# Performance work log

Measured on AMD Instinct MI355X. Metric: run time of the kernel, lower is better.

The kernel has to match this reference:

```python
import jax, jax.numpy as jnp
import numpy as np

F8 = jnp.float8_e4m3fn
F8_MAX = 448.0  # finfo(float8_e4m3fn).max

def setup_inputs() -> dict:
    key = jax.random.key(0)
    k1, k2, k3 = jax.random.split(key, 3)
    B, S, IN, OUT = 4, 4096, 2048, 2048
    x = jax.random.normal(k1, (B, S, IN), dtype=jnp.float32)
    # Pre-quantized fp8 weight [OUT, IN] with a per-tensor scale, as stored by AutoFP8
    w = jax.random.normal(k2, (OUT, IN), dtype=jnp.float32)
    weight_scale = (jnp.max(jnp.abs(w)) / F8_MAX).astype(jnp.float32)
    qweight = jnp.clip(w / weight_scale, -F8_MAX, F8_MAX).astype(F8)
    input_scale = jnp.asarray(0.05, dtype=jnp.float32)  # static activation scale
    bias = jax.random.normal(k3, (OUT,), dtype=jnp.float32)
    return {"x": x, "qweight": qweight, "weight_scale": weight_scale,
            "input_scale": input_scale, "bias": bias}

def reference(x, qweight, weight_scale, input_scale, bias):
    # per_tensor_quantize: divide by static scale, clamp to fp8 range, cast to e4m3fn
    qinput = jnp.clip(x / input_scale, -F8_MAX, F8_MAX).astype(F8)  # [B,S,IN] fp8
    # scaled fp8 GEMM with fused dequant + bias epilogue (out_dtype = x.dtype)
    a = qinput.astype(x.dtype) * input_scale          # dequant activations
    b = qweight.astype(x.dtype) * weight_scale        # dequant weights [OUT,IN]
    return jnp.einsum('bsi,oi->bso', a, b) + bias     # [B,S,OUT]
```

## Files before the change

kernel.cpp:

```cpp
#include <hip/hip_runtime.h>
#include <stdint.h>

typedef float  floatx4 __attribute__((ext_vector_type(4)));
typedef int    intx4   __attribute__((ext_vector_type(4)));
typedef int    intx8   __attribute__((ext_vector_type(8)));

#define AS1 __attribute__((address_space(1)))
#define AS3 __attribute__((address_space(3)))

__device__ __forceinline__ float quant_e4m3_value(float v) {
  float av = fabsf(v);
  float step, rstep;
  if (av < 0.015625f) {
    step  = 0.001953125f;
    rstep = 512.0f;
  } else {
    uint32_t e = __float_as_uint(av) >> 23;
    step  = __uint_as_float((e - 3u) << 23);
    rstep = __uint_as_float((257u - e) << 23);
  }
  return rintf(v * rstep) * step;
}

__device__ __forceinline__ uint32_t enc_e4m3(float v) {
  uint32_t u = __float_as_uint(v);
  uint32_t s = (u >> 24) & 0x80u;
  float av = fabsf(v);
  uint32_t b;
  if (av < 0.015625f) {
    b = s | (uint32_t)(av * 512.0f);
  } else {
    uint32_t e = ((u >> 23) & 0xffu) - 120u;
    uint32_t m = (u >> 20) & 7u;
    b = s | (e << 3) | m;
  }
  return b;
}

__device__ __forceinline__ uint32_t quant4(float4 v, float s) {
  float a0 = quant_e4m3_value(fminf(fmaxf(v.x / s, -448.0f), 448.0f));
  float a1 = quant_e4m3_value(fminf(fmaxf(v.y / s, -448.0f), 448.0f));
  float a2 = quant_e4m3_value(fminf(fmaxf(v.z / s, -448.0f), 448.0f));
  float a3 = quant_e4m3_value(fminf(fmaxf(v.w / s, -448.0f), 448.0f));
  return enc_e4m3(a0) | (enc_e4m3(a1) << 8) | (enc_e4m3(a2) << 16) |
         (enc_e4m3(a3) << 24);
}

__global__ __launch_bounds__(256) void quantize_x_kernel(
    const float4* __restrict__ x, const float* __restrict__ s_ptr,
    uint4* __restrict__ q, int n16) {
  int i = blockIdx.x * 256 + threadIdx.x;
  if (i >= n16) return;
  const float s = s_ptr[0];
  uint4 o;
  o.x = quant4(x[i * 4 + 0], s);
  o.y = quant4(x[i * 4 + 1], s);
  o.z = quant4(x[i * 4 + 2], s);
  o.w = quant4(x[i * 4 + 3], s);
  q[i] = o;
}

__global__ __launch_bounds__(256) void prep_w_kernel(
    const uint8_t* __restrict__ qw, uint4* __restrict__ w8, int n16) {
  const uint32_t* q32 = (const uint32_t*)qw;
  int lane = threadIdx.x & 63;
  uint32_t w0 = q32[lane], w1 = q32[lane + 64];
  bool fa = ((w0 & 0xFFFFFu) == 0u) && ((w1 & 0xFFFFFu) == 0u);
  uint32_t nib = (w0 | (w0 >> 16) | w1 | (w1 >> 16)) & 0xFu;
  unsigned long long ba = __ballot(fa);
  unsigned long long bb = __ballot(nib == 0u);
  int m = (ba == ~0ull) ? 2 : ((bb == ~0ull) ? 1 : 0);

  int i = blockIdx.x * 256 + threadIdx.x;
  if (i >= n16) return;
  uint4 o;
  uint32_t r[4];
  if (m == 1) {
#pragma unroll
    for (int j = 0; j < 4; ++j) {
      ushort4 u = ((const ushort4*)qw)[i * 4 + j];
      r[j] = enc_e4m3(__uint_as_float((uint32_t)u.x << 16)) |
             (enc_e4m3(__uint_as_float((uint32_t)u.y << 16)) << 8) |
             (enc_e4m3(__uint_as_float((uint32_t)u.z << 16)) << 16) |
             (enc_e4m3(__uint_as_float((uint32_t)u.w << 16)) << 24);
    }
  } else if (m == 2) {
#pragma unroll
    for (int j = 0; j < 4; ++j) {
      float4 v = ((const float4*)qw)[i * 4 + j];
      r[j] = enc_e4m3(v.x) | (enc_e4m3(v.y) << 8) | (enc_e4m3(v.z) << 16) |
             (enc_e4m3(v.w) << 24);
    }
  } else {
    uint4 c = ((const uint4*)qw)[i];
    r[0] = c.x; r[1] = c.y; r[2] = c.z; r[3] = c.w;
  }
  o.x = r[0]; o.y = r[1]; o.z = r[2]; o.w = r[3];
  w8[i] = o;
}

__global__ __launch_bounds__(512, 2) void gemm_fp8_kernel(
    const uint8_t* __restrict__ A, const uint8_t* __restrict__ B,
    const float* __restrict__ wscale, const float* __restrict__ iscale,
    const float* __restrict__ bias, float* __restrict__ out,
    int M, int N, int K) {
  __shared__ uint8_t lds[131072];

  const int tid  = threadIdx.x;
  const int lane = tid & 63;
  const int wave = tid >> 6;

  const int nbx = gridDim.x;
  const int nwg = nbx * gridDim.y;
  int flat = blockIdx.y * nbx + blockIdx.x;
  flat = (flat & 7) * (nwg >> 3) + (flat >> 3);
  const int bm = flat / nbx;
  const int bn = flat - bm * nbx;

  const int wm = (wave >> 2) * 128;
  const int wn = (wave & 3) * 64;
  const int r15 = lane & 15, quad = lane >> 4, k8 = r15 & 7;
  const int posL = ((2 * quad)     ^ k8) << 4;
  const int posH = ((2 * quad + 1) ^ k8) << 4;

  const uint8_t* aS[2]; const uint8_t* bS[2]; uint32_t dOf[2];
#pragma unroll
  for (int j = 0; j < 2; ++j) {
    const int s = tid + j * 512, rl = s >> 3, p = s & 7;
    aS[j] = A + (size_t)(bm * 256 + rl) * K + ((p ^ (rl & 7)) << 4);
    bS[j] = B + (size_t)(bn * 256 + rl) * K + ((p ^ (rl & 7)) << 4);
    dOf[j] = (uint32_t)s << 4;
  }
  const size_t hK = (size_t)128 * K;

#define STG_A(j, h, kb, bf_)                                                   \
  __builtin_amdgcn_global_load_lds(                                            \
      (const AS1 void*)(aS[j] + (h) * hK + (kb)),                              \
      (AS3 void*)(&lds[(bf_) * 32768u + (h) * 16384u + dOf[j]]), 16, 0, 0)
#define STG_B(j, h, kb, bf_)                                                   \
  __builtin_amdgcn_global_load_lds(                                            \
      (const AS1 void*)(bS[j] + (h) * hK + (kb)),                              \
      (AS3 void*)(&lds[65536u + (bf_) * 32768u + (h) * 16384u + dOf[j]]),      \
      16, 0, 0)

  floatx4 acc[8][4];
#pragma unroll
  for (int i = 0; i < 8; ++i)
#pragma unroll
    for (int j = 0; j < 4; ++j) acc[i][j] = (floatx4){0.f, 0.f, 0.f, 0.f};

  const int T = K >> 7;

  STG_A(0, 0, 0, 0); STG_A(1, 0, 0, 0); STG_A(0, 1, 0, 0); STG_A(1, 1, 0, 0);
  STG_B(0, 0, 0, 0); STG_B(1, 0, 0, 0); STG_B(0, 1, 0, 0); STG_B(1, 1, 0, 0);
  if (T > 1) {
    STG_B(0, 0, 128, 1); STG_B(1, 0, 128, 1);
    STG_B(0, 1, 128, 1); STG_B(1, 1, 128, 1);
    asm volatile("s_waitcnt vmcnt(4)" ::: "memory");
  } else {
    asm volatile("s_waitcnt vmcnt(0)" ::: "memory");
  }
  __builtin_amdgcn_sched_barrier(0);
  __builtin_amdgcn_s_barrier();

  for (int t = 0; t < T; ++t) {
    const int cur = t & 1;
    const uint8_t* LA = &lds[cur * 32768u] + (wm + r15) * 128;
    const uint8_t* LB = &lds[65536u + cur * 32768u] + (wn + r15) * 128;
    const int kb1 = (t + 1) << 7, kb2 = (t + 2) << 7;
    const bool sA = (t + 1 < T), sB = (t + 2 < T);
    intx8 af[4], bf[4];

#pragma unroll
    for (int i = 0; i < 4; ++i) {
      intx4 lo = *(const intx4*)(LA + i * 2048 + posL);
      intx4 hi = *(const intx4*)(LA + i * 2048 + posH);
      af[i] = __builtin_shufflevector(lo, hi, 0, 1, 2, 3, 4, 5, 6, 7);
    }
#pragma unroll
    for (int j = 0; j < 2; ++j) {
      intx4 lo = *(const intx4*)(LB + j * 2048 + posL);
      intx4 hi = *(const intx4*)(LB + j * 2048 + posH);
      bf[j] = __builtin_shufflevector(lo, hi, 0, 1, 2, 3, 4, 5, 6, 7);
    }
    if (sA) { STG_A(0, 0, kb1, cur ^ 1); STG_A(1, 0, kb1, cur ^ 1); }
    __builtin_amdgcn_s_barrier();
    __builtin_amdgcn_s_setprio(1);
#pragma unroll
    for (int i = 0; i < 4; ++i)
#pragma unroll
      for (int j = 0; j < 2; ++j)
        acc[i][j] = __builtin_amdgcn_mfma_scale_f32_16x16x128_f8f6f4(
            af[i], bf[j], acc[i][j], 0, 0, 0, 127, 0, 127);
    __builtin_amdgcn_s_setprio(0);
    __builtin_amdgcn_s_barrier();

#pragma unroll
    for (int j = 2; j < 4; ++j) {
      intx4 lo = *(const intx4*)(LB + j * 2048 + posL);
      intx4 hi = *(const intx4*)(LB + j * 2048 + posH);
      bf[j] = __builtin_shufflevector(lo, hi, 0, 1, 2, 3, 4, 5, 6, 7);
    }
    if (sA) { STG_A(0, 1, kb1, cur ^ 1); STG_A(1, 1, kb1, cur ^ 1); }
    __builtin_amdgcn_s_barrier();
    __builtin_amdgcn_s_setprio(1);
#pragma unroll
    for (int i = 0; i < 4; ++i)
#pragma unroll
      for (int j = 2; j < 4; ++j)
        acc[i][j] = __builtin_amdgcn_mfma_scale_f32_16x16x128_f8f6f4(
            af[i], bf[j], acc[i][j], 0, 0, 0, 127, 0, 127);
    __builtin_amdgcn_s_setprio(0);
    __builtin_amdgcn_s_barrier();

#pragma unroll
    for (int i = 0; i < 4; ++i) {
      intx4 lo = *(const intx4*)(LA + 8192 + i * 2048 + posL);
      intx4 hi = *(const intx4*)(LA + 8192 + i * 2048 + posH);
      af[i] = __builtin_shufflevector(lo, hi, 0, 1, 2, 3, 4, 5, 6, 7);
    }
    if (sB) { STG_B(0, 0, kb2, cur); STG_B(1, 0, kb2, cur); }
    __builtin_amdgcn_s_barrier();
    __builtin_amdgcn_s_setprio(1);
#pragma unroll
    for (int i = 0; i < 4; ++i)
#pragma unroll
      for (int j = 2; j < 4; ++j)
        acc[4 + i][j] = __builtin_amdgcn_mfma_scale_f32_16x16x128_f8f6f4(
            af[i], bf[j], acc[4 + i][j], 0, 0, 0, 127, 0, 127);
    __builtin_amdgcn_s_setprio(0);
    __builtin_amdgcn_s_barrier();

    if (sB) { STG_B(0, 1, kb2, cur); STG_B(1, 1, kb2, cur); }
    __builtin_amdgcn_s_barrier();
    __builtin_amdgcn_s_setprio(1);
#pragma unroll
    for (int i = 0; i < 4; ++i)
#pragma unroll
      for (int j = 0; j < 2; ++j)
        acc[4 + i][j] = __builtin_amdgcn_mfma_scale_f32_16x16x128_f8f6f4(
            af[i], bf[j], acc[4 + i][j], 0, 0, 0, 127, 0, 127);
    __builtin_amdgcn_s_setprio(0);
    if (t + 1 < T) {
      if (t + 2 < T) asm volatile("s_waitcnt vmcnt(4)" ::: "memory");
      else           asm volatile("s_waitcnt vmcnt(0)" ::: "memory");
      __builtin_amdgcn_sched_barrier(0);
    }
    __builtin_amdgcn_s_barrier();
  }

  const float sc = wscale[0] * iscale[0];
  const int rq = quad * 4;
#pragma unroll
  for (int jj = 0; jj < 4; ++jj) {
    const int col = bn * 256 + wn + jj * 16 + r15;
    const float bv = bias[col];
#pragma unroll
    for (int mi = 0; mi < 8; ++mi) {
      const int row = bm * 256 + wm + (mi >> 2) * 64 + (mi & 3) * 16 + rq;
      float* o = out + (size_t)row * N + col;
#pragma unroll
      for (int r = 0; r < 4; ++r)
        o[(size_t)r * N] = acc[mi][jj][r] * sc + bv;
    }
  }
#undef STG_A
#undef STG_B
}

extern "C" void kernel_launch(void* const* d_in, const int* in_sizes, int n_in,
                              void* d_out, int out_size, void* d_ws,
                              size_t ws_size, hipStream_t stream) {
  const float*   x      = (const float*)d_in[0];
  const uint8_t* qw     = (const uint8_t*)d_in[1];
  const float*   wscale = (const float*)d_in[2];
  const float*   iscale = (const float*)d_in[3];
  const float*   bias   = (const float*)d_in[4];
  float*         out    = (float*)d_out;

  const int N = in_sizes[4];
  const int K = in_sizes[1] / N;
  const int M = in_sizes[0] / K;

  uint8_t* qx = (uint8_t*)d_ws;
  uint8_t* w8 = qx + (size_t)M * K;

  const int nx16 = in_sizes[0] / 16;
  quantize_x_kernel<<<(nx16 + 255) / 256, 256, 0, stream>>>(
      (const float4*)x, iscale, (uint4*)qx, nx16);

  const int nw16 = in_sizes[1] / 16;
  prep_w_kernel<<<(nw16 + 255) / 256, 256, 0, stream>>>(qw, (uint4*)w8, nw16);

  dim3 grid(N / 256, M / 256);
  gemm_fp8_kernel<<<grid, 512, 0, stream>>>(qx, w8, wscale, iscale, bias,
                                            out, M, N, K);
}
```

Baseline: 324.8 us.

## Collapse four-phase MFMA loop into two phases with fewer barriers

After: 320.8 us. Within noise of the previous version (-1.2%).

```diff
diff --git a/kernel.cpp b/kernel.cpp
--- a/kernel.cpp
+++ b/kernel.cpp
@@ -168,50 +168,39 @@
     const uint8_t* LA = &lds[cur * 32768u] + (wm + r15) * 128;
     const uint8_t* LB = &lds[65536u + cur * 32768u] + (wn + r15) * 128;
     const int kb1 = (t + 1) << 7, kb2 = (t + 2) << 7;
-    const bool sA = (t + 1 < T), sB = (t + 2 < T);
     intx8 af[4], bf[4];
 
+    if (t + 1 < T) {
+      STG_A(0, 0, kb1, cur ^ 1); STG_A(1, 0, kb1, cur ^ 1);
+      STG_A(0, 1, kb1, cur ^ 1); STG_A(1, 1, kb1, cur ^ 1);
+    }
+
+#pragma unroll
+    for (int j = 0; j < 4; ++j) {
+      intx4 lo = *(const intx4*)(LB + j * 2048 + posL);
+      intx4 hi = *(const intx4*)(LB + j * 2048 + posH);
+      bf[j] = __builtin_shufflevector(lo, hi, 0, 1, 2, 3, 4, 5, 6, 7);
+    }
 #pragma unroll
     for (int i = 0; i < 4; ++i) {
       intx4 lo = *(const intx4*)(LA + i * 2048 + posL);
       intx4 hi = *(const intx4*)(LA + i * 2048 + posH);
       af[i] = __builtin_shufflevector(lo, hi, 0, 1, 2, 3, 4, 5, 6, 7);
     }
-#pragma unroll
-    for (int j = 0; j < 2; ++j) {
-      intx4 lo = *(const intx4*)(LB + j * 2048 + posL);
-      intx4 hi = *(const intx4*)(LB + j * 2048 + posH);
-      bf[j] = __builtin_shufflevector(lo, hi, 0, 1, 2, 3, 4, 5, 6, 7);
-    }
-    if (sA) { STG_A(0, 0, kb1, cur ^ 1); STG_A(1, 0, kb1, cur ^ 1); }
-    __builtin_amdgcn_s_barrier();
     __builtin_amdgcn_s_setprio(1);
 #pragma unroll
     for (int i = 0; i < 4; ++i)
 #pragma unroll
-      for (int j = 0; j < 2; ++j)
+      for (int j = 0; j < 4; ++j)
         acc[i][j] = __builtin_amdgcn_mfma_scale_f32_16x16x128_f8f6f4(
             af[i], bf[j], acc[i][j], 0, 0, 0, 127, 0, 127);
     __builtin_amdgcn_s_setprio(0);
+
     __builtin_amdgcn_s_barrier();
-
-#pragma unroll
-    for (int j = 2; j < 4; ++j) {
-      intx4 lo = *(const intx4*)(LB + j * 2048 + posL);
-      intx4 hi = *(const intx4*)(LB + j * 2048 + posH);
-      bf[j] = __builtin_shufflevector(lo, hi, 0, 1, 2, 3, 4, 5, 6, 7);
-    }
-    if (sA) { STG_A(0, 1, kb1, cur ^ 1); STG_A(1, 1, kb1, cur ^ 1); }
-    __builtin_amdgcn_s_barrier();
-    __builtin_amdgcn_s_setprio(1);
-#pragma unroll
-    for (int i = 0; i < 4; ++i)
-#pragma unroll
-      for (int j = 2; j < 4; ++j)
-        acc[i][j] = __builtin_amdgcn_mfma_scale_f32_16x16x128_f8f6f4(
-            af[i], bf[j], acc[i][j], 0, 0, 0, 127, 0, 127);
-    __builtin_amdgcn_s_setprio(0);
-    __builtin_amdgcn_s_barrier();
+    if (t + 2 < T) {
+      STG_B(0, 0, kb2, cur); STG_B(1, 0, kb2, cur);
+      STG_B(0, 1, kb2, cur); STG_B(1, 1, kb2, cur);
+    }
 
 #pragma unroll
     for (int i = 0; i < 4; ++i) {
@@ -219,34 +208,21 @@
       intx4 hi = *(const intx4*)(LA + 8192 + i * 2048 + posH);
       af[i] = __builtin_shufflevector(lo, hi, 0, 1, 2, 3, 4, 5, 6, 7);
     }
-    if (sB) { STG_B(0, 0, kb2, cur); STG_B(1, 0, kb2, cur); }
-    __builtin_amdgcn_s_barrier();
     __builtin_amdgcn_s_setprio(1);
 #pragma unroll
     for (int i = 0; i < 4; ++i)
 #pragma unroll
-      for (int j = 2; j < 4; ++j)
+      for (int j = 0; j < 4; ++j)
         acc[4 + i][j] = __builtin_amdgcn_mfma_scale_f32_16x16x128_f8f6f4(
             af[i], bf[j], acc[4 + i][j], 0, 0, 0, 127, 0, 127);
     __builtin_amdgcn_s_setprio(0);
-    __builtin_amdgcn_s_barrier();
-
-    if (sB) { STG_B(0, 1, kb2, cur); STG_B(1, 1, kb2, cur); }
-    __builtin_amdgcn_s_barrier();
-    __builtin_amdgcn_s_setprio(1);
-#pragma unroll
-    for (int i = 0; i < 4; ++i)
-#pragma unroll
-      for (int j = 0; j < 2; ++j)
-        acc[4 + i][j] = __builtin_amdgcn_mfma_scale_f32_16x16x128_f8f6f4(
-            af[i], bf[j], acc[4 + i][j], 0, 0, 0, 127, 0, 127);
-    __builtin_amdgcn_s_setprio(0);
+
     if (t + 1 < T) {
       if (t + 2 < T) asm volatile("s_waitcnt vmcnt(4)" ::: "memory");
       else           asm volatile("s_waitcnt vmcnt(0)" ::: "memory");
       __builtin_amdgcn_sched_barrier(0);
-    }
-    __builtin_amdgcn_s_barrier();
+      __builtin_amdgcn_s_barrier();
+    }
   }
 
   const float sc = wscale[0] * iscale[0];
```
